# Kernel tuning notes

Measured on AMD Instinct MI355X. Metric: run time of the kernel, lower is better.

## Reference

```python
import jax, jax.numpy as jnp
import numpy as np
from functools import partial

DN = jax.lax.conv_dimension_numbers((1, 1, 3, 3), (1, 1, 3, 3), ('NCHW', 'OIHW', 'NCHW'))


def setup_inputs() -> dict:
    key = jax.random.key(0)
    ks = jax.random.split(key, 5)
    x = jax.random.normal(ks[0], (16, 1, 512, 512), dtype=jnp.float32)
    k = jax.random.normal(ks[1], (1, 1, 3, 3), dtype=jnp.float32)
    w1 = jax.random.normal(ks[2], (10, 1), dtype=jnp.float32) * 0.5
    b1 = jax.random.normal(ks[3], (10,), dtype=jnp.float32) * 0.1
    w2 = jax.random.normal(ks[4], (1, 10), dtype=jnp.float32) * 0.5
    return {"x": x, "k": k, "w1": w1, "b1": b1, "w2": w2, "steps": 16}


def _step(x, k, w1, b1, w2):
    # 3x3 stencil, 1 channel, SAME padding, no bias
    out = jax.lax.conv_general_dilated(x, k, (1, 1), 'SAME', dimension_numbers=DN)
    # gaussian activation
    out = jnp.exp(-(out - 1.0) ** 2)
    # pointwise MLP: 1 -> 10 (ReLU) -> 1 (Sigmoid)
    h = jax.nn.relu(jnp.einsum('bchw,oc->bohw', out, w1) + b1[None, :, None, None])
    out = jax.nn.sigmoid(jnp.einsum('bchw,oc->bohw', h, w2))
    # residual update
    return x + (out - 0.5)


def reference(x, k, w1, b1, w2, steps):
    def body(x, _):
        x_new = _step(x, k, w1, b1, w2)
        return x_new, x_new

    _, seq = jax.lax.scan(body, x, None, length=steps)
    # prepend initial state: [steps+1, B, 1, H, W]
    return jnp.concatenate([x[None], seq], axis=0)
```

## Files before the change

### kernel.cpp

```cpp
#include <hip/hip_runtime.h>


#define NCA_H 512
#define NCA_W 512
#define NCA_HW (NCA_H * NCA_W)
#define TX 80
#define HALO 8
#define NG 20
#define NACT 240

__global__ __launch_bounds__(256) void nca_fused(float* __restrict__ traj,
                                                 size_t slice,
                                                 int nsteps,
                                                 const float* __restrict__ kc,
                                                 const float* __restrict__ w1v,
                                                 const float* __restrict__ b1v,
                                                 const float* __restrict__ w2v) {
    __shared__ float buf[2][TX * TX];

    float kk[9];
#pragma unroll
    for (int i = 0; i < 9; ++i) kk[i] = kc[i];
    float rw1[10], rb1[10], rw2[10];
#pragma unroll
    for (int o = 0; o < 10; ++o) { rw1[o] = w1v[o]; rb1[o] = b1v[o]; rw2[o] = w2v[o]; }

    const int bi = blockIdx.x;
    const int b  = bi >> 6;
    const int ty = (bi >> 3) & 7;
    const int tx = bi & 7;
    const int gh0 = ty * 64 - HALO;
    const int gw0 = tx * 64 - HALO;

    const float* sp = traj + (size_t)b * NCA_HW;
    for (int i = threadIdx.x; i < (TX * TX / 4); i += 256) {
        int row = i / NG;
        int c4  = i - row * NG;
        int gh  = gh0 + row;
        int gw  = gw0 + 4 * c4;
        float4 v = make_float4(0.f, 0.f, 0.f, 0.f);
        if (((unsigned)gh < NCA_H) && ((unsigned)gw < NCA_W))
            v = *(const float4*)(sp + (size_t)gh * NCA_W + gw);
        *(float4*)&buf[0][row * TX + 4 * c4] = v;
    }
    if (threadIdx.x < 2 * NG) {
        int row = (threadIdx.x < NG) ? 0 : (TX - 1);
        int c4  = threadIdx.x % NG;
        *(float4*)&buf[1][row * TX + 4 * c4] = make_float4(0.f, 0.f, 0.f, 0.f);
    }
    __syncthreads();

    const int tid = threadIdx.x;
    const bool active = tid < NACT;
    const int g  = tid % NG;
    const int rb = tid / NG;
    const int w0 = g * 4;
    const int r0 = (rb < 6) ? (1 + 7 * rb) : (43 + 6 * (rb - 6));
    const int r1 = r0 + ((rb < 6) ? 7 : 6);
    const bool colStore = active && (w0 >= HALO) && (w0 < TX - HALO);
    const bool colIn = ((unsigned)(gw0 + w0) < NCA_W);
    const int wl = (w0 > 0) ? (w0 - 1) : 0;
    const int wr = (w0 + 4 < TX) ? (w0 + 4) : (TX - 1);

    int cur = 0;
    for (int s = 1; s <= nsteps; ++s) {
        const float* cb = buf[cur];
        float* nb = buf[cur ^ 1];
        float* gout = traj + (size_t)s * slice + (size_t)b * NCA_HW;
        if (active) {
            for (int r = r0; r < r1; ++r) {
                const bool ok = colIn && ((unsigned)(gh0 + r) < NCA_H);
                float rv[3][6];
#pragma unroll
                for (int rr = 0; rr < 3; ++rr) {
                    const float* rp = cb + (r - 1 + rr) * TX;
                    float4 c4v = *(const float4*)(rp + w0);
                    rv[rr][0] = rp[wl];
                    rv[rr][1] = c4v.x; rv[rr][2] = c4v.y;
                    rv[rr][3] = c4v.z; rv[rr][4] = c4v.w;
                    rv[rr][5] = rp[wr];
                }
                float4 res;
                float* resp = (float*)&res;
#pragma unroll
                for (int j = 0; j < 4; ++j) {
                    float sacc = 0.f;
#pragma unroll
                    for (int rr = 0; rr < 3; ++rr) {
                        sacc = fmaf(kk[rr * 3 + 0], rv[rr][j],     sacc);
                        sacc = fmaf(kk[rr * 3 + 1], rv[rr][j + 1], sacc);
                        sacc = fmaf(kk[rr * 3 + 2], rv[rr][j + 2], sacc);
                    }
                    float d = sacc - 1.0f;
                    float gg = __expf(-d * d);
                    float acc = 0.f;
#pragma unroll
                    for (int o = 0; o < 10; ++o) {
                        float hm = fmaxf(fmaf(rw1[o], gg, rb1[o]), 0.f);
                        acc = fmaf(rw2[o], hm, acc);
                    }
                    float sig = __fdividef(1.0f, 1.0f + __expf(-acc));
                    float val = rv[1][j + 1] + (sig - 0.5f);
                    resp[j] = ok ? val : 0.f;
                }
                *(float4*)&nb[r * TX + w0] = res;
                if (colStore && r >= HALO && r < TX - HALO)
                    *(float4*)(gout + (size_t)(gh0 + r) * NCA_W + (gw0 + w0)) = res;
            }
        }
        __syncthreads();
        cur ^= 1;
    }
}

extern "C" void kernel_launch(void* const* d_in, const int* in_sizes, int n_in,
                              void* d_out, int out_size, void* d_ws, size_t ws_size,
                              hipStream_t stream) {
    const float* x  = (const float*)d_in[0];
    const float* k  = (const float*)d_in[1];
    const float* w1 = (const float*)d_in[2];
    const float* b1 = (const float*)d_in[3];
    const float* w2 = (const float*)d_in[4];
    float* out = (float*)d_out;

    const size_t slice = (size_t)in_sizes[0];
    const int steps = out_size / (int)slice - 1;
    const int B = (int)(slice / NCA_HW);

    hipMemcpyAsync(out, x, slice * sizeof(float), hipMemcpyDeviceToDevice, stream);

    const int blocks = B * 64;
    for (int base = 0; base < steps; base += HALO) {
        int ns = steps - base;
        if (ns > HALO) ns = HALO;
        nca_fused<<<blocks, 256, 0, stream>>>(out + (size_t)base * slice, slice, ns,
                                              k, w1, b1, w2);
    }
}
```

Baseline: 480.0 us.

## Reuse stencil rows in registers with wave shuffles and fuse initial copy

Each thread now keeps a rolling window of four register rows across its strip of output rows, so each shared-memory row is loaded once rather than three times. Left and right neighbours come from wave shuffles instead of extra scalar LDS reads. Threads are remapped so each 64-lane wave holds three 20-lane row groups, with four idle lanes per wave. The separate device-to-device copy of the initial state is folded into the first kernel launch's tile load, and launch bounds now request three blocks per SM. Risk: shuffles at the edge of each 20-lane group read a lane from the neighbouring group rather than the clamped value, which changes results only in halo columns that are never stored.

```diff
diff --git a/kernel.cpp b/kernel.cpp
--- a/kernel.cpp
+++ b/kernel.cpp
@@ -7,15 +7,53 @@
 #define TX 80
 #define HALO 8
 #define NG 20
-#define NACT 240
 
-__global__ __launch_bounds__(256) void nca_fused(float* __restrict__ traj,
-                                                 size_t slice,
-                                                 int nsteps,
-                                                 const float* __restrict__ kc,
-                                                 const float* __restrict__ w1v,
-                                                 const float* __restrict__ b1v,
-                                                 const float* __restrict__ w2v) {
+#define LOADR(W, rrow) do {                                                  \
+    const float4 q_ = *(const float4*)(cb + (rrow) * TX + w0);               \
+    W[1] = q_.x; W[2] = q_.y; W[3] = q_.z; W[4] = q_.w;                      \
+    W[0] = __shfl_up(q_.w, 1);                                               \
+    W[5] = __shfl_down(q_.x, 1);                                             \
+} while (0)
+
+#define COMPR(Wm, Wc, Wp, rrow) do {                                         \
+    const int rr_ = (rrow);                                                  \
+    const bool ok_ = colIn && ((unsigned)(gh0 + rr_) < NCA_H);               \
+    float4 res_; float* rp_ = (float*)&res_;                                 \
+    _Pragma("unroll")                                                        \
+    for (int j = 0; j < 4; ++j) {                                            \
+        float s_ = 0.f;                                                      \
+        s_ = fmaf(kk[0], Wm[j],     s_);                                     \
+        s_ = fmaf(kk[1], Wm[j + 1], s_);                                     \
+        s_ = fmaf(kk[2], Wm[j + 2], s_);                                     \
+        s_ = fmaf(kk[3], Wc[j],     s_);                                     \
+        s_ = fmaf(kk[4], Wc[j + 1], s_);                                     \
+        s_ = fmaf(kk[5], Wc[j + 2], s_);                                     \
+        s_ = fmaf(kk[6], Wp[j],     s_);                                     \
+        s_ = fmaf(kk[7], Wp[j + 1], s_);                                     \
+        s_ = fmaf(kk[8], Wp[j + 2], s_);                                     \
+        float d_ = s_ - 1.0f;                                                \
+        float g_ = __expf(-d_ * d_);                                         \
+        float a_ = 0.f;                                                      \
+        _Pragma("unroll")                                                    \
+        for (int o = 0; o < 10; ++o) {                                       \
+            float h_ = fmaxf(fmaf(rw1[o], g_, rb1[o]), 0.f);                 \
+            a_ = fmaf(rw2[o], h_, a_);                                       \
+        }                                                                    \
+        float sg_ = __fdividef(1.0f, 1.0f + __expf(-a_));                    \
+        float v_ = Wc[j + 1] + (sg_ - 0.5f);                                 \
+        rp_[j] = ok_ ? v_ : 0.f;                                             \
+    }                                                                        \
+    *(float4*)&nb[rr_ * TX + w0] = res_;                                     \
+    if (colStore && rr_ >= HALO && rr_ < TX - HALO)                          \
+        *(float4*)(gout + (size_t)(gh0 + rr_) * NCA_W + (gw0 + w0)) = res_;  \
+} while (0)
+
+__global__ __launch_bounds__(256, 3) void nca_fused(
+        const float* __restrict__ src,
+        float* __restrict__ traj,
+        size_t slice, int nsteps, int writeInit,
+        const float* __restrict__ kc, const float* __restrict__ w1v,
+        const float* __restrict__ b1v, const float* __restrict__ w2v) {
     __shared__ float buf[2][TX * TX];
 
     float kk[9];
@@ -32,7 +70,8 @@
     const int gh0 = ty * 64 - HALO;
     const int gw0 = tx * 64 - HALO;
 
-    const float* sp = traj + (size_t)b * NCA_HW;
+    const float* sp = src + (size_t)b * NCA_HW;
+    float* ip = traj + (size_t)b * NCA_HW;
     for (int i = threadIdx.x; i < (TX * TX / 4); i += 256) {
         int row = i / NG;
         int c4  = i - row * NG;
@@ -41,7 +80,10 @@
         float4 v = make_float4(0.f, 0.f, 0.f, 0.f);
         if (((unsigned)gh < NCA_H) && ((unsigned)gw < NCA_W))
             v = *(const float4*)(sp + (size_t)gh * NCA_W + gw);
-        *(float4*)&buf[0][row * TX + 4 * c4] = v;
+        *(float4*)&buf[0][4 * i] = v;
+        if (writeInit && row >= HALO && row < TX - HALO &&
+            c4 >= (HALO / 4) && c4 < (TX - HALO) / 4)
+            *(float4*)(ip + (size_t)gh * NCA_W + gw) = v;
     }
     if (threadIdx.x < 2 * NG) {
         int row = (threadIdx.x < NG) ? 0 : (TX - 1);
@@ -50,17 +92,17 @@
     }
     __syncthreads();
 
-    const int tid = threadIdx.x;
-    const bool active = tid < NACT;
-    const int g  = tid % NG;
-    const int rb = tid / NG;
-    const int w0 = g * 4;
-    const int r0 = (rb < 6) ? (1 + 7 * rb) : (43 + 6 * (rb - 6));
-    const int r1 = r0 + ((rb < 6) ? 7 : 6);
+    const int tid  = threadIdx.x;
+    const int lane = tid & 63;
+    const int wid  = tid >> 6;
+    const bool active = lane < 60;
+    const int g    = lane % 20;
+    const int sidx = wid * 3 + lane / 20;
+    const int w0   = g * 4;
+    const int r0   = (sidx < 6) ? (1 + 7 * sidx) : (43 + 6 * (sidx - 6));
+    const bool n7  = (sidx < 6);
     const bool colStore = active && (w0 >= HALO) && (w0 < TX - HALO);
     const bool colIn = ((unsigned)(gw0 + w0) < NCA_W);
-    const int wl = (w0 > 0) ? (w0 - 1) : 0;
-    const int wr = (w0 + 4 < TX) ? (w0 + 4) : (TX - 1);
 
     int cur = 0;
     for (int s = 1; s <= nsteps; ++s) {
@@ -68,45 +110,16 @@
         float* nb = buf[cur ^ 1];
         float* gout = traj + (size_t)s * slice + (size_t)b * NCA_HW;
         if (active) {
-            for (int r = r0; r < r1; ++r) {
-                const bool ok = colIn && ((unsigned)(gh0 + r) < NCA_H);
-                float rv[3][6];
-#pragma unroll
-                for (int rr = 0; rr < 3; ++rr) {
-                    const float* rp = cb + (r - 1 + rr) * TX;
-                    float4 c4v = *(const float4*)(rp + w0);
-                    rv[rr][0] = rp[wl];
-                    rv[rr][1] = c4v.x; rv[rr][2] = c4v.y;
-                    rv[rr][3] = c4v.z; rv[rr][4] = c4v.w;
-                    rv[rr][5] = rp[wr];
-                }
-                float4 res;
-                float* resp = (float*)&res;
-#pragma unroll
-                for (int j = 0; j < 4; ++j) {
-                    float sacc = 0.f;
-#pragma unroll
-                    for (int rr = 0; rr < 3; ++rr) {
-                        sacc = fmaf(kk[rr * 3 + 0], rv[rr][j],     sacc);
-                        sacc = fmaf(kk[rr * 3 + 1], rv[rr][j + 1], sacc);
-                        sacc = fmaf(kk[rr * 3 + 2], rv[rr][j + 2], sacc);
-                    }
-                    float d = sacc - 1.0f;
-                    float gg = __expf(-d * d);
-                    float acc = 0.f;
-#pragma unroll
-                    for (int o = 0; o < 10; ++o) {
-                        float hm = fmaxf(fmaf(rw1[o], gg, rb1[o]), 0.f);
-                        acc = fmaf(rw2[o], hm, acc);
-                    }
-                    float sig = __fdividef(1.0f, 1.0f + __expf(-acc));
-                    float val = rv[1][j + 1] + (sig - 0.5f);
-                    resp[j] = ok ? val : 0.f;
-                }
-                *(float4*)&nb[r * TX + w0] = res;
-                if (colStore && r >= HALO && r < TX - HALO)
-                    *(float4*)(gout + (size_t)(gh0 + r) * NCA_W + (gw0 + w0)) = res;
-            }
+            float A[6], B[6], C[6], D[6];
+            LOADR(A, r0 - 1); LOADR(B, r0);
+            LOADR(C, r0 + 1); LOADR(D, r0 + 2);
+            COMPR(A, B, C, r0);       LOADR(A, r0 + 3);
+            COMPR(B, C, D, r0 + 1);   LOADR(B, r0 + 4);
+            COMPR(C, D, A, r0 + 2);   LOADR(C, r0 + 5);
+            COMPR(D, A, B, r0 + 3);   LOADR(D, r0 + 6);
+            COMPR(A, B, C, r0 + 4);
+            COMPR(B, C, D, r0 + 5);
+            if (n7) { LOADR(A, r0 + 7); COMPR(C, D, A, r0 + 6); }
         }
         __syncthreads();
         cur ^= 1;
@@ -127,13 +140,13 @@
     const int steps = out_size / (int)slice - 1;
     const int B = (int)(slice / NCA_HW);
 
-    hipMemcpyAsync(out, x, slice * sizeof(float), hipMemcpyDeviceToDevice, stream);
-
     const int blocks = B * 64;
     for (int base = 0; base < steps; base += HALO) {
         int ns = steps - base;
         if (ns > HALO) ns = HALO;
-        nca_fused<<<blocks, 256, 0, stream>>>(out + (size_t)base * slice, slice, ns,
+        const float* s0 = (base == 0) ? x : (out + (size_t)base * slice);
+        nca_fused<<<blocks, 256, 0, stream>>>(s0, out + (size_t)base * slice,
+                                              slice, ns, (base == 0) ? 1 : 0,
                                               k, w1, b1, w2);
     }
 }
```

Result: faster. 453.6 us (-5.5%).
